# Kernel optimization log

Hardware: AMD Instinct MI355X
Metric: run time of the kernel (lower is better)

## Reference

```python
import jax, jax.numpy as jnp
import numpy as np

N_NODES = 50000
N_EDGES = 800000
IN_DIM = 64
HID = 128
N_LAYERS = 3
NEG_SLOPE = 0.2  # PyG GATConv default


def setup_inputs() -> dict:
    key = jax.random.key(0)
    ks = jax.random.split(key, 24)

    def lin(kw, kb, fan_in, fan_out):
        bound = 1.0 / np.sqrt(fan_in)
        W = jax.random.uniform(kw, (fan_out, fan_in), jnp.float32, -bound, bound)
        b = jax.random.uniform(kb, (fan_out,), jnp.float32, -bound, bound)
        return W, b

    x = jax.random.normal(ks[0], (N_NODES, IN_DIM), jnp.float32)
    h = jax.random.normal(ks[1], (N_NODES, HID), jnp.float32)
    edge_index = jax.random.randint(ks[2], (2, N_EDGES), 0, N_NODES, jnp.int64)

    W_enc, b_enc = lin(ks[3], ks[4], IN_DIM + HID, HID)

    # GAT layer params, stacked over layers: W [L,H,H], att vectors [L,H], bias [L,H]
    Wg = jnp.stack([lin(ks[5 + i], ks[8 + i], HID, HID)[0] for i in range(N_LAYERS)])
    att_src = jax.random.normal(ks[11], (N_LAYERS, HID), jnp.float32) * (1.0 / np.sqrt(HID))
    att_dst = jax.random.normal(ks[12], (N_LAYERS, HID), jnp.float32) * (1.0 / np.sqrt(HID))
    bg = jnp.zeros((N_LAYERS, HID), jnp.float32)

    Wd, bd = lin(ks[13], ks[14], 2 * HID, HID)
    Wd1, bd1 = lin(ks[15], ks[16], HID, HID)
    Wh, bh = lin(ks[17], ks[18], HID, 1)
    Wt, bt = lin(ks[19], ks[20], HID, 1)

    return dict(x=x, h=h, edge_index=edge_index, W_enc=W_enc, b_enc=b_enc,
                Wg=Wg, att_src=att_src, att_dst=att_dst, bg=bg,
                Wd=Wd, bd=bd, Wd1=Wd1, bd1=bd1, Wh=Wh, bh=bh, Wt=Wt, bt=bt)


def _gat_conv(xf, src, dst, W, a_s, a_d, b, n_nodes):
    # xf: [N,H]; messages flow src -> dst, softmax over incoming edges of dst
    xw = xf @ W.T                                   # [N,H]
    e = jax.nn.leaky_relu((xw @ a_s)[src] + (xw @ a_d)[dst], NEG_SLOPE)  # [E]
    m = jax.ops.segment_max(e, dst, num_segments=n_nodes)
    ex = jnp.exp(e - m[dst])
    denom = jax.ops.segment_sum(ex, dst, num_segments=n_nodes)
    alpha = ex / denom[dst]                         # [E]
    out = jax.ops.segment_sum(xw[src] * alpha[:, None], dst, num_segments=n_nodes)
    return out + b


def reference(x, h, edge_index, W_enc, b_enc, Wg, att_src, att_dst, bg,
              Wd, bd, Wd1, bd1, Wh, bh, Wt, bt):
    n = x.shape[0]
    # Encoder
    z = jnp.concatenate([x, h], axis=1) @ W_enc.T + b_enc   # [N,H]

    # add self-loops (PyG GATConv default add_self_loops=True)
    loops = jnp.arange(n, dtype=edge_index.dtype)
    src = jnp.concatenate([edge_index[0], loops])
    dst = jnp.concatenate([edge_index[1], loops])

    # GAT processor: relu(conv_i) for all layers, then last conv applied again (no relu)
    out = z
    for i in range(Wg.shape[0]):
        out = jax.nn.relu(_gat_conv(out, src, dst, Wg[i], att_src[i], att_dst[i], bg[i], n))
    hL = _gat_conv(out, src, dst, Wg[-1], att_src[-1], att_dst[-1], bg[-1], n)

    # Decoder (BatchNorm1d is defined but unused in the original forward)
    d = jax.nn.relu(jnp.concatenate([hL, z], axis=1) @ Wd.T + bd)
    d = jax.nn.relu(d @ Wd1.T + bd1)
    y = jax.nn.sigmoid(d @ Wh.T + bh)                        # [N,1]

    # Termination
    h_bar = jnp.mean(hL, axis=0)                             # [H]
    t = jax.nn.sigmoid(h_bar @ Wt.T + bt)                    # [1]
    return (y, t, hL)
```

## Files before the change

kernel.cpp:

```cpp
#include <hip/hip_runtime.h>

#define N_NODES 50000
#define N_EDGES 800000
#define E_TOT   (N_EDGES + N_NODES)
#define HID     128

typedef unsigned short u16;
typedef unsigned int   u32;
typedef __bf16 bf16x8 __attribute__((ext_vector_type(8)));
typedef float  f32x4  __attribute__((ext_vector_type(4)));

__device__ __forceinline__ float b2f(u16 u) {
  union { u32 i; float f; } c; c.i = ((u32)u) << 16; return c.f;
}
__device__ __forceinline__ u16 f2b(float f) {
  union { float f; u32 i; } c; c.f = f;
  u32 u = c.i;
  return (u16)((u + 0x7fffu + ((u >> 16) & 1u)) >> 16);
}


__global__ void k_detect(const void* x, const void* ei, int* flags) {
  int lane = threadIdx.x;
  const u16* xw = (const u16*)x;
  int wildF = 0;
  #pragma unroll
  for (int i = 0; i < 4; ++i) {
    u16 w = xw[lane + 64 * i];
    int e = (w >> 7) & 0xff;
    if (e >= 0x89) wildF = 1;
  }
  unsigned long long bF = __ballot(wildF);
  const int* e32 = (const int*)ei;
  int nzOdd = 0;
  #pragma unroll
  for (int i = 0; i < 2; ++i)
    if (e32[2 * (lane + 64 * i) + 1] != 0) nzOdd = 1;
  unsigned long long bI = __ballot(nzOdd);
  if (lane == 0) {
    flags[0] = (bF != 0ull) ? 1 : 0;
    flags[1] = (bI != 0ull) ? 0 : 1;
  }
}


__global__ __launch_bounds__(256) void k_convert(
    const void* Wenc, const void* Wg, const void* Wd, const void* Wd1,
    const void* benc, const void* bg, const void* atts, const void* attd,
    const void* bd, const void* bd1, const void* Wh, const void* bh,
    const void* Wt, const void* bt,
    u16* WencH, u16* WencL, u16* WgH, u16* WgL, u16* WdH, u16* WdL,
    u16* Wd1H, u16* Wd1L, float* vecf, const int* flags)
{
  int isF32 = flags[0];
  int t = blockIdx.x * 256 + threadIdx.x;
  auto ld = [&](const void* p, int i) -> float {
    return isF32 ? ((const float*)p)[i] : b2f(((const u16*)p)[i]);
  };
  auto sp = [&](u16* H, u16* L, int i, float v) {
    u16 hh = f2b(v); H[i] = hh; L[i] = f2b(v - b2f(hh));
  };
  if      (t < 24576)  { sp(WencH, WencL, t, ld(Wenc, t)); }
  else if (t < 73728)  { int i = t - 24576;  sp(WgH,  WgL,  i, ld(Wg, i)); }
  else if (t < 106496) { int i = t - 73728;  sp(WdH,  WdL,  i, ld(Wd, i)); }
  else if (t < 122880) { int i = t - 106496; sp(Wd1H, Wd1L, i, ld(Wd1, i)); }
  else if (t < 123008) { int i = t - 122880; vecf[i]        = ld(benc, i); }
  else if (t < 123392) { int i = t - 123008; vecf[128 + i]  = ld(bg, i); }
  else if (t < 123776) { int i = t - 123392; vecf[512 + i]  = ld(atts, i); }
  else if (t < 124160) { int i = t - 123776; vecf[896 + i]  = ld(attd, i); }
  else if (t < 124288) { int i = t - 124160; vecf[1280 + i] = ld(bd, i); }
  else if (t < 124416) { int i = t - 124288; vecf[1408 + i] = ld(bd1, i); }
  else if (t < 124544) { int i = t - 124416; vecf[1536 + i] = ld(Wh, i); }
  else if (t == 124544) { vecf[1664] = ld(bh, 0); }
  else if (t < 124673) { int i = t - 124545; vecf[1665 + i] = ld(Wt, i); }
  else if (t == 124673) { vecf[1793] = ld(bt, 0); }
}


__device__ __forceinline__ int ld_ei(const int* ei, size_t idx, int i64) {
  int v = i64 ? (int)((const long long*)ei)[idx] : ei[idx];
  return ((unsigned)v < (unsigned)N_NODES) ? v : 0;
}

__global__ void k_deg(const int* __restrict__ ei, int* __restrict__ deg, const int* flags) {
  int i64 = flags[1];
  int k = blockIdx.x * 256 + threadIdx.x;
  if (k >= E_TOT) return;
  int d = (k < N_EDGES) ? ld_ei(ei, (size_t)N_EDGES + k, i64) : (k - N_EDGES);
  atomicAdd(&deg[d], 1);
}

__device__ __forceinline__ int block_scan_excl(int v, int lane, int w, int* wsum, int& total) {
  int x = v;
  #pragma unroll
  for (int d = 1; d < 64; d <<= 1) {
    int y = __shfl_up(x, d);
    if (lane >= d) x += y;
  }
  if (lane == 63) wsum[w] = x;
  __syncthreads();
  int wOff = 0;
  #pragma unroll
  for (int i = 0; i < 4; ++i) wOff += (i < w) ? wsum[i] : 0;
  total = wsum[0] + wsum[1] + wsum[2] + wsum[3];
  return wOff + x - v;
}

__global__ void k_scan_block(const int* __restrict__ in, int* __restrict__ outExcl,
                             int* __restrict__ blkSum, int n, int* __restrict__ totalOut) {
  __shared__ int wsum[4];
  int t = threadIdx.x, lane = t & 63, w = t >> 6;
  int gid = blockIdx.x * 256 + t;
  int v = (gid < n) ? in[gid] : 0;
  int total;
  int excl = block_scan_excl(v, lane, w, wsum, total);
  if (gid < n) outExcl[gid] = excl;
  if (t == 0) {
    if (blkSum)   blkSum[blockIdx.x] = total;
    if (totalOut) totalOut[0] = total;
  }
}

__global__ void k_scan_add(int* __restrict__ rowp, const int* __restrict__ blkOff,
                           int* __restrict__ cursor, int n) {
  int gid = blockIdx.x * 256 + threadIdx.x;
  if (gid < n) {
    int r = rowp[gid] + blkOff[blockIdx.x];
    rowp[gid] = r;
    cursor[gid] = r;
  }
}

__global__ void k_scatter(const int* __restrict__ ei, int* __restrict__ cursor,
                          int* __restrict__ colsrc, const int* flags) {
  int i64 = flags[1];
  int k = blockIdx.x * 256 + threadIdx.x;
  if (k >= E_TOT) return;
  int s, d;
  if (k < N_EDGES) { s = ld_ei(ei, k, i64); d = ld_ei(ei, (size_t)N_EDGES + k, i64); }
  else             { s = d = k - N_EDGES; }
  int pos = atomicAdd(&cursor[d], 1);
  colsrc[pos] = s;
}


__device__ __forceinline__ void loadSplit8(const float* p, bf16x8& hi, bf16x8& lo) {
  union { u16 a[8]; bf16x8 v; } H, L;
  #pragma unroll
  for (int i = 0; i < 8; ++i) {
    float v = p[i];
    u16 hh = f2b(v);
    H.a[i] = hh;
    L.a[i] = f2b(v - b2f(hh));
  }
  hi = H.v; lo = L.v;
}

__global__ __launch_bounds__(256) void k_gemm(
    const void* A1a, const void* A1b, int s1, int K1,
    const void* A2a, const void* A2b, int s2,
    const u16* __restrict__ WH, const u16* __restrict__ WL,
    const float* __restrict__ biasF,
    float* __restrict__ outF_, u16* __restrict__ outH, u16* __restrict__ outL,
    const float* __restrict__ asv, const float* __restrict__ adv,
    float* __restrict__ ssrc, float* __restrict__ sdst,
    int N, int K, int relu, int aMode, const int* flags)
{
  int isF32 = flags[0];
  int wid  = blockIdx.x * 4 + (threadIdx.x >> 6);
  int lane = threadIdx.x & 63;
  int q = lane >> 4, c = lane & 15;
  int nb = wid * 32;
  if (nb >= N) return;
  f32x4 acc[2][8] = {};
  int r0 = nb + c;      if (r0 > N - 1) r0 = N - 1;
  int r1 = nb + 16 + c; if (r1 > N - 1) r1 = N - 1;

  for (int kb = 0; kb < K; kb += 32) {
    int kf = kb + q * 8;
    bf16x8 a0h, a1h, a0l, a1l;
    if (aMode == 1) {
      const void* Ap; int stride, ks;
      if (kf < K1) { Ap = A1a; stride = s1; ks = kf; }
      else         { Ap = A2a; stride = s2; ks = kf - K1; }
      if (isF32) {
        loadSplit8((const float*)Ap + (size_t)r0 * stride + ks, a0h, a0l);
        loadSplit8((const float*)Ap + (size_t)r1 * stride + ks, a1h, a1l);
      } else {
        union { u16 u[8]; bf16x8 v; } Z = {};
        a0h = *(const bf16x8*)((const u16*)Ap + (size_t)r0 * stride + ks);
        a1h = *(const bf16x8*)((const u16*)Ap + (size_t)r1 * stride + ks);
        a0l = Z.v; a1l = Z.v;
      }
    } else {
      const u16 *PH, *PL; int stride, ks;
      if (kf < K1) { PH = (const u16*)A1a; PL = (const u16*)A1b; stride = s1; ks = kf; }
      else         { PH = (const u16*)A2a; PL = (const u16*)A2b; stride = s2; ks = kf - K1; }
      a0h = *(const bf16x8*)(PH + (size_t)r0 * stride + ks);
      a0l = *(const bf16x8*)(PL + (size_t)r0 * stride + ks);
      a1h = *(const bf16x8*)(PH + (size_t)r1 * stride + ks);
      a1l = *(const bf16x8*)(PL + (size_t)r1 * stride + ks);
    }
    const u16* wph = WH + (size_t)c * K + kb + q * 8;
    const u16* wpl = WL + (size_t)c * K + kb + q * 8;
    #pragma unroll
    for (int ct = 0; ct < 8; ++ct) {
      bf16x8 bh_ = *(const bf16x8*)(wph + (size_t)(ct * 16) * K);
      bf16x8 bl_ = *(const bf16x8*)(wpl + (size_t)(ct * 16) * K);
      acc[0][ct] = __builtin_amdgcn_mfma_f32_16x16x32_bf16(a0h, bh_, acc[0][ct], 0, 0, 0);
      acc[1][ct] = __builtin_amdgcn_mfma_f32_16x16x32_bf16(a1h, bh_, acc[1][ct], 0, 0, 0);
      acc[0][ct] = __builtin_amdgcn_mfma_f32_16x16x32_bf16(a0h, bl_, acc[0][ct], 0, 0, 0);
      acc[1][ct] = __builtin_amdgcn_mfma_f32_16x16x32_bf16(a1h, bl_, acc[1][ct], 0, 0, 0);
      acc[0][ct] = __builtin_amdgcn_mfma_f32_16x16x32_bf16(a0l, bh_, acc[0][ct], 0, 0, 0);
      acc[1][ct] = __builtin_amdgcn_mfma_f32_16x16x32_bf16(a1l, bh_, acc[1][ct], 0, 0, 0);
    }
  }

  #pragma unroll
  for (int ct = 0; ct < 8; ++ct) {
    int col = ct * 16 + c;
    float bv = biasF ? biasF[col] : 0.0f;
    #pragma unroll
    for (int g = 0; g < 2; ++g) {
      #pragma unroll
      for (int r = 0; r < 4; ++r) {
        float vv = acc[g][ct][r] + bv;
        if (relu) vv = fmaxf(vv, 0.0f);
        acc[g][ct][r] = vv;
        int node = nb + g * 16 + q * 4 + r;
        if (node < N) {
          size_t o = (size_t)node * HID + col;
          if (outF_) outF_[o] = vv;
          if (outH) {
            u16 hh = f2b(vv);
            outH[o] = hh;
            outL[o] = f2b(vv - b2f(hh));
          }
        }
      }
    }
  }

  if (asv) {
    #pragma unroll
    for (int g = 0; g < 2; ++g) {
      #pragma unroll
      for (int r = 0; r < 4; ++r) {
        float ssum = 0.0f, dsum = 0.0f;
        #pragma unroll
        for (int ct = 0; ct < 8; ++ct) {
          int col = ct * 16 + c;
          float v = acc[g][ct][r];
          ssum += v * asv[col];
          dsum += v * adv[col];
        }
        #pragma unroll
        for (int m = 1; m < 16; m <<= 1) {
          ssum += __shfl_xor(ssum, m);
          dsum += __shfl_xor(dsum, m);
        }
        int node = nb + g * 16 + q * 4 + r;
        if (c == 0 && node < N) { ssrc[node] = ssum; sdst[node] = dsum; }
      }
    }
  }
}


__global__ __launch_bounds__(256) void k_softmax(const int* __restrict__ rowp,
    const int* __restrict__ colsrc, const float* __restrict__ ssrc,
    const float* __restrict__ sdst, float* __restrict__ alpha)
{
  int node = blockIdx.x * 4 + (threadIdx.x >> 6);
  int lane = threadIdx.x & 63;
  int start = rowp[node], end = rowp[node + 1];
  float sdv = sdst[node];
  float mx = -1e30f;
  for (int j = start + lane; j < end; j += 64) {
    float e = ssrc[colsrc[j]] + sdv;
    e = (e >= 0.0f) ? e : 0.2f * e;
    alpha[j] = e;
    mx = fmaxf(mx, e);
  }
  #pragma unroll
  for (int d = 1; d < 64; d <<= 1) mx = fmaxf(mx, __shfl_xor(mx, d));
  float sum = 0.0f;
  for (int j = start + lane; j < end; j += 64) {
    float ex = __expf(alpha[j] - mx);
    alpha[j] = ex;
    sum += ex;
  }
  #pragma unroll
  for (int d = 1; d < 64; d <<= 1) sum += __shfl_xor(sum, d);
  float inv = 1.0f / sum;
  for (int j = start + lane; j < end; j += 64) alpha[j] *= inv;
}


__global__ __launch_bounds__(256) void k_gather(const int* __restrict__ rowp,
    const int* __restrict__ colsrc, const float* __restrict__ alpha,
    const float* __restrict__ xw, const float* __restrict__ biasF,
    u16* __restrict__ outH, u16* __restrict__ outL,
    float* __restrict__ out2, int relu)
{
  int node = blockIdx.x * 4 + (threadIdx.x >> 6);
  int lane = threadIdx.x & 63;
  int half = lane >> 5, hl = lane & 31;
  int start = rowp[node], end = rowp[node + 1];
  float a0 = 0, a1 = 0, a2 = 0, a3 = 0;
  for (int j0 = start; j0 < end; j0 += 8) {
    int idx = j0 + (lane & 7);
    bool ok = idx < end;
    int   sI = ok ? colsrc[idx] : 0;
    float aI = ok ? alpha[idx]  : 0.0f;
    #pragma unroll
    for (int t = 0; t < 8; t += 2) {
      int   ss = __shfl(sI, t + half);
      float aa = __shfl(aI, t + half);
      float4 p = *(const float4*)(xw + (size_t)ss * HID + hl * 4);
      a0 += aa * p.x; a1 += aa * p.y; a2 += aa * p.z; a3 += aa * p.w;
    }
  }
  a0 += __shfl_xor(a0, 32); a1 += __shfl_xor(a1, 32);
  a2 += __shfl_xor(a2, 32); a3 += __shfl_xor(a3, 32);
  if (half == 0) {
    int col = hl * 4;
    float4 b = *(const float4*)(biasF + col);
    a0 += b.x; a1 += b.y; a2 += b.z; a3 += b.w;
    if (relu) { a0 = fmaxf(a0, 0.f); a1 = fmaxf(a1, 0.f); a2 = fmaxf(a2, 0.f); a3 = fmaxf(a3, 0.f); }
    size_t o = (size_t)node * HID + col;
    u16 h0 = f2b(a0), h1 = f2b(a1), h2 = f2b(a2), h3 = f2b(a3);
    ushort4 hv; hv.x = h0; hv.y = h1; hv.z = h2; hv.w = h3;
    *(ushort4*)(outH + o) = hv;
    ushort4 lv;
    lv.x = f2b(a0 - b2f(h0)); lv.y = f2b(a1 - b2f(h1));
    lv.z = f2b(a2 - b2f(h2)); lv.w = f2b(a3 - b2f(h3));
    *(ushort4*)(outL + o) = lv;
    if (out2) { out2[o] = a0; out2[o + 1] = a1; out2[o + 2] = a2; out2[o + 3] = a3; }
  }
}


__global__ __launch_bounds__(256) void k_hbar(const u16* __restrict__ hH, const u16* __restrict__ hLo,
                                              float* __restrict__ hbar) {
  int t = threadIdx.x;
  int col = t & 127, g = t >> 7;
  float acc = 0.0f;
  for (int n = blockIdx.x * 2 + g; n < N_NODES; n += gridDim.x * 2) {
    size_t o = (size_t)n * HID + col;
    acc += b2f(hH[o]) + b2f(hLo[o]);
  }
  atomicAdd(&hbar[col], acc);
}


__global__ __launch_bounds__(256) void k_ydot(const float* __restrict__ d2,
    const float* __restrict__ Whf, const float* __restrict__ bhf, float* __restrict__ yout)
{
  int node = blockIdx.x * 4 + (threadIdx.x >> 6);
  int lane = threadIdx.x & 63;
  float2 p = *(const float2*)(d2 + (size_t)node * HID + lane * 2);
  float v = p.x * Whf[lane * 2] + p.y * Whf[lane * 2 + 1];
  #pragma unroll
  for (int d = 1; d < 64; d <<= 1) v += __shfl_xor(v, d);
  if (lane == 0) {
    float s = 1.0f / (1.0f + __expf(-(v + bhf[0])));
    yout[node] = s;
  }
}


__global__ void k_tker(const float* __restrict__ hbar, const float* __restrict__ Wtf,
                       const float* __restrict__ btf, float* __restrict__ tout) {
  int lane = threadIdx.x;
  float v = hbar[lane] * Wtf[lane] + hbar[lane + 64] * Wtf[lane + 64];
  #pragma unroll
  for (int d = 1; d < 64; d <<= 1) v += __shfl_xor(v, d);
  if (lane == 0) {
    float t = 1.0f / (1.0f + __expf(-(v * (1.0f / N_NODES) + btf[0])));
    tout[0] = t;
  }
}


extern "C" void kernel_launch(void* const* d_in, const int* in_sizes, int n_in,
                              void* d_out, int out_size, void* d_ws, size_t ws_size,
                              hipStream_t stream) {
  const void* x    = d_in[0];
  const void* h    = d_in[1];
  const int*  ei   = (const int*)d_in[2];
  const void* Wenc = d_in[3];
  const void* benc = d_in[4];
  const void* Wg   = d_in[5];
  const void* atts = d_in[6];
  const void* attd = d_in[7];
  const void* bg   = d_in[8];
  const void* Wd   = d_in[9];
  const void* bd   = d_in[10];
  const void* Wd1  = d_in[11];
  const void* bd1v = d_in[12];
  const void* Wh   = d_in[13];
  const void* bh   = d_in[14];
  const void* Wt   = d_in[15];
  const void* bt   = d_in[16];
  float* outF = (float*)d_out;

  char* w = (char*)d_ws;
  auto alloc = [&](size_t bytes) { char* p = w; w += (bytes + 255) & ~(size_t)255; return p; };
  const size_t NPLANE = (size_t)N_NODES * HID;
  float* xwF    = (float*)alloc(NPLANE * 4);
  u16*   zH     = (u16*)  alloc(NPLANE * 2);
  u16*   zL     = (u16*)  alloc(NPLANE * 2);
  u16*   aH     = (u16*)  alloc(NPLANE * 2);
  u16*   aL     = (u16*)  alloc(NPLANE * 2);
  float* ssrc   = (float*)alloc((size_t)N_NODES * 4);
  float* sdst   = (float*)alloc((size_t)N_NODES * 4);
  int*   deg    = (int*)  alloc((size_t)N_NODES * 4);
  int*   rowp   = (int*)  alloc((size_t)(N_NODES + 1) * 4);
  int*   cursor = (int*)  alloc((size_t)N_NODES * 4);
  int*   colsrc = (int*)  alloc((size_t)E_TOT * 4);
  float* alpha  = (float*)alloc((size_t)E_TOT * 4);
  int*   blkSum = (int*)  alloc(1024);
  int*   blkOff = (int*)  alloc(1024);
  float* hbar   = (float*)alloc(512);
  int*   flags  = (int*)  alloc(256);
  u16*   WencH  = (u16*)  alloc(24576 * 2);
  u16*   WencL  = (u16*)  alloc(24576 * 2);
  u16*   WgH    = (u16*)  alloc(49152 * 2);
  u16*   WgL    = (u16*)  alloc(49152 * 2);
  u16*   WdH    = (u16*)  alloc(32768 * 2);
  u16*   WdL    = (u16*)  alloc(32768 * 2);
  u16*   Wd1H   = (u16*)  alloc(16384 * 2);
  u16*   Wd1L   = (u16*)  alloc(16384 * 2);
  float* vecf   = (float*)alloc(2048 * 4);
  u16*   dH     = (u16*)xwF;
  u16*   dL     = dH + NPLANE;
  float* d2F    = (float*)aH;

  const int NODE_BLKS = N_NODES / 4;
  const int EDGE_BLKS = (E_TOT + 255) / 256;
  const int SCAN_BLKS = (N_NODES + 255) / 256;
  const int GEMM_BLKS = ((N_NODES + 31) / 32 + 3) / 4;
  const int CONV_BLKS = (124674 + 255) / 256;

  k_detect<<<1, 64, 0, stream>>>(x, ei, flags);
  k_convert<<<CONV_BLKS, 256, 0, stream>>>(Wenc, Wg, Wd, Wd1, benc, bg, atts, attd,
                                           bd, bd1v, Wh, bh, Wt, bt,
                                           WencH, WencL, WgH, WgL, WdH, WdL,
                                           Wd1H, Wd1L, vecf, flags);

  hipMemsetAsync(deg, 0, (size_t)N_NODES * 4, stream);
  hipMemsetAsync(hbar, 0, 128 * sizeof(float), stream);
  k_deg<<<EDGE_BLKS, 256, 0, stream>>>(ei, deg, flags);
  k_scan_block<<<SCAN_BLKS, 256, 0, stream>>>(deg, rowp, blkSum, N_NODES, nullptr);
  k_scan_block<<<1, 256, 0, stream>>>(blkSum, blkOff, nullptr, SCAN_BLKS, rowp + N_NODES);
  k_scan_add<<<SCAN_BLKS, 256, 0, stream>>>(rowp, blkOff, cursor, N_NODES);
  k_scatter<<<EDGE_BLKS, 256, 0, stream>>>(ei, cursor, colsrc, flags);

  k_gemm<<<GEMM_BLKS, 256, 0, stream>>>(x, nullptr, 64, 64, h, nullptr, HID,
                                        WencH, WencL, vecf,
                                        nullptr, zH, zL,
                                        nullptr, nullptr, nullptr, nullptr,
                                        N_NODES, 192, 0, 1, flags);

  for (int l4 = 0; l4 < 4; ++l4) {
    int l = (l4 < 3) ? l4 : 2;
    int relu = (l4 < 3) ? 1 : 0;
    const u16* inH = (l4 == 0) ? zH : aH;
    const u16* inL = (l4 == 0) ? zL : aL;
    k_gemm<<<GEMM_BLKS, 256, 0, stream>>>(inH, inL, HID, HID, nullptr, nullptr, HID,
                                          WgH + (size_t)l * HID * HID, WgL + (size_t)l * HID * HID,
                                          nullptr,
                                          xwF, nullptr, nullptr,
                                          vecf + 512 + l * HID, vecf + 896 + l * HID, ssrc, sdst,
                                          N_NODES, HID, 0, 2, flags);
    k_softmax<<<NODE_BLKS, 256, 0, stream>>>(rowp, colsrc, ssrc, sdst, alpha);
    k_gather<<<NODE_BLKS, 256, 0, stream>>>(rowp, colsrc, alpha, xwF, vecf + 128 + l * HID,
                                            aH, aL, (l4 == 3) ? (outF + N_NODES + 1) : nullptr, relu);
  }

  k_hbar<<<256, 256, 0, stream>>>(aH, aL, hbar);

  k_gemm<<<GEMM_BLKS, 256, 0, stream>>>(aH, aL, HID, HID, zH, zL, HID,
                                        WdH, WdL, vecf + 1280,
                                        nullptr, dH, dL,
                                        nullptr, nullptr, nullptr, nullptr,
                                        N_NODES, 256, 1, 2, flags);
  k_gemm<<<GEMM_BLKS, 256, 0, stream>>>(dH, dL, HID, HID, nullptr, nullptr, HID,
                                        Wd1H, Wd1L, vecf + 1408,
                                        d2F, nullptr, nullptr,
                                        nullptr, nullptr, nullptr, nullptr,
                                        N_NODES, 128, 1, 2, flags);
  k_ydot<<<NODE_BLKS, 256, 0, stream>>>(d2F, vecf + 1536, vecf + 1664, outF);
  k_tker<<<1, 64, 0, stream>>>(hbar, vecf + 1665, vecf + 1793, outF + N_NODES);
}
```

Measured before the change: 782.9 us.

## Precompute W^T·att vectors and fuse attention scores into gather epilogue

Result: slower. 844.8 us (+7.9%).

```diff
diff --git a/kernel.cpp b/kernel.cpp
--- a/kernel.cpp
+++ b/kernel.cpp
@@ -77,6 +77,21 @@
 }
 
 
+__global__ void k_wa(const u16* __restrict__ WgH, const u16* __restrict__ WgL,
+                     const float* __restrict__ vecf, float* __restrict__ waS, float* __restrict__ waD) {
+  int t = blockIdx.x * 256 + threadIdx.x;
+  if (t >= 768) return;
+  int l = t / 256, sel = (t / 128) & 1, k = t & 127;
+  const float* av = vecf + (sel ? 896 : 512) + l * HID;
+  const u16* H = WgH + (size_t)l * HID * HID;
+  const u16* L = WgL + (size_t)l * HID * HID;
+  float s = 0.0f;
+  for (int c = 0; c < HID; ++c)
+    s += (b2f(H[(size_t)c * HID + k]) + b2f(L[(size_t)c * HID + k])) * av[c];
+  (sel ? waD : waS)[l * HID + k] = s;
+}
+
+
 __device__ __forceinline__ int ld_ei(const int* ei, size_t idx, int i64) {
   int v = i64 ? (int)((const long long*)ei)[idx] : ei[idx];
   return ((unsigned)v < (unsigned)N_NODES) ? v : 0;
@@ -162,8 +177,6 @@
     const u16* __restrict__ WH, const u16* __restrict__ WL,
     const float* __restrict__ biasF,
     float* __restrict__ outF_, u16* __restrict__ outH, u16* __restrict__ outL,
-    const float* __restrict__ asv, const float* __restrict__ adv,
-    float* __restrict__ ssrc, float* __restrict__ sdst,
     int N, int K, int relu, int aMode, const int* flags)
 {
   int isF32 = flags[0];
@@ -226,7 +239,6 @@
       for (int r = 0; r < 4; ++r) {
         float vv = acc[g][ct][r] + bv;
         if (relu) vv = fmaxf(vv, 0.0f);
-        acc[g][ct][r] = vv;
         int node = nb + g * 16 + q * 4 + r;
         if (node < N) {
           size_t o = (size_t)node * HID + col;
@@ -240,30 +252,25 @@
       }
     }
   }
-
-  if (asv) {
-    #pragma unroll
-    for (int g = 0; g < 2; ++g) {
-      #pragma unroll
-      for (int r = 0; r < 4; ++r) {
-        float ssum = 0.0f, dsum = 0.0f;
-        #pragma unroll
-        for (int ct = 0; ct < 8; ++ct) {
-          int col = ct * 16 + c;
-          float v = acc[g][ct][r];
-          ssum += v * asv[col];
-          dsum += v * adv[col];
-        }
-        #pragma unroll
-        for (int m = 1; m < 16; m <<= 1) {
-          ssum += __shfl_xor(ssum, m);
-          dsum += __shfl_xor(dsum, m);
-        }
-        int node = nb + g * 16 + q * 4 + r;
-        if (c == 0 && node < N) { ssrc[node] = ssum; sdst[node] = dsum; }
-      }
-    }
-  }
+}
+
+
+__global__ __launch_bounds__(256) void k_sdots(const u16* __restrict__ zH, const u16* __restrict__ zL,
+    const float* __restrict__ waS0, const float* __restrict__ waD0,
+    float* __restrict__ ssrc, float* __restrict__ sdst)
+{
+  int node = blockIdx.x * 4 + (threadIdx.x >> 6);
+  int lane = threadIdx.x & 63;
+  size_t o = (size_t)node * HID + lane * 2;
+  u32 ph = *(const u32*)(zH + o);
+  u32 pl = *(const u32*)(zL + o);
+  float v0 = b2f((u16)ph) + b2f((u16)pl);
+  float v1 = b2f((u16)(ph >> 16)) + b2f((u16)(pl >> 16));
+  float vs = v0 * waS0[lane * 2] + v1 * waS0[lane * 2 + 1];
+  float vd = v0 * waD0[lane * 2] + v1 * waD0[lane * 2 + 1];
+  #pragma unroll
+  for (int d = 1; d < 64; d <<= 1) { vs += __shfl_xor(vs, d); vd += __shfl_xor(vd, d); }
+  if (lane == 0) { ssrc[node] = vs; sdst[node] = vd; }
 }
 
 
@@ -301,20 +308,23 @@
     const int* __restrict__ colsrc, const float* __restrict__ alpha,
     const float* __restrict__ xw, const float* __restrict__ biasF,
     u16* __restrict__ outH, u16* __restrict__ outL,
-    float* __restrict__ out2, int relu)
+    float* __restrict__ out2,
+    const float* __restrict__ waSn, const float* __restrict__ waDn,
+    float* __restrict__ ssrc, float* __restrict__ sdst, int relu)
 {
   int node = blockIdx.x * 4 + (threadIdx.x >> 6);
   int lane = threadIdx.x & 63;
   int half = lane >> 5, hl = lane & 31;
   int start = rowp[node], end = rowp[node + 1];
   float a0 = 0, a1 = 0, a2 = 0, a3 = 0;
-  for (int j0 = start; j0 < end; j0 += 8) {
-    int idx = j0 + (lane & 7);
+  for (int j0 = start; j0 < end; j0 += 16) {
+    int idx = j0 + (lane & 15);
     bool ok = idx < end;
     int   sI = ok ? colsrc[idx] : 0;
     float aI = ok ? alpha[idx]  : 0.0f;
     #pragma unroll
-    for (int t = 0; t < 8; t += 2) {
+    for (int t = 0; t < 16; t += 2) {
+      if (j0 + t >= end) break;
       int   ss = __shfl(sI, t + half);
       float aa = __shfl(aI, t + half);
       float4 p = *(const float4*)(xw + (size_t)ss * HID + hl * 4);
@@ -323,11 +333,11 @@
   }
   a0 += __shfl_xor(a0, 32); a1 += __shfl_xor(a1, 32);
   a2 += __shfl_xor(a2, 32); a3 += __shfl_xor(a3, 32);
+  int col = hl * 4;
+  float4 b = *(const float4*)(biasF + col);
+  a0 += b.x; a1 += b.y; a2 += b.z; a3 += b.w;
+  if (relu) { a0 = fmaxf(a0, 0.f); a1 = fmaxf(a1, 0.f); a2 = fmaxf(a2, 0.f); a3 = fmaxf(a3, 0.f); }
   if (half == 0) {
-    int col = hl * 4;
-    float4 b = *(const float4*)(biasF + col);
-    a0 += b.x; a1 += b.y; a2 += b.z; a3 += b.w;
-    if (relu) { a0 = fmaxf(a0, 0.f); a1 = fmaxf(a1, 0.f); a2 = fmaxf(a2, 0.f); a3 = fmaxf(a3, 0.f); }
     size_t o = (size_t)node * HID + col;
     u16 h0 = f2b(a0), h1 = f2b(a1), h2 = f2b(a2), h3 = f2b(a3);
     ushort4 hv; hv.x = h0; hv.y = h1; hv.z = h2; hv.w = h3;
@@ -337,6 +347,15 @@
     lv.z = f2b(a2 - b2f(h2)); lv.w = f2b(a3 - b2f(h3));
     *(ushort4*)(outL + o) = lv;
     if (out2) { out2[o] = a0; out2[o + 1] = a1; out2[o + 2] = a2; out2[o + 3] = a3; }
+  }
+  if (waSn) {
+    float4 ws = *(const float4*)(waSn + col);
+    float4 wd = *(const float4*)(waDn + col);
+    float vs = a0 * ws.x + a1 * ws.y + a2 * ws.z + a3 * ws.w;
+    float vd = a0 * wd.x + a1 * wd.y + a2 * wd.z + a3 * wd.w;
+    #pragma unroll
+    for (int d = 1; d < 32; d <<= 1) { vs += __shfl_xor(vs, d); vd += __shfl_xor(vd, d); }
+    if (lane == 0) { ssrc[node] = vs; sdst[node] = vd; }
   }
 }
 
@@ -433,6 +452,8 @@
   u16*   Wd1H   = (u16*)  alloc(16384 * 2);
   u16*   Wd1L   = (u16*)  alloc(16384 * 2);
   float* vecf   = (float*)alloc(2048 * 4);
+  float* waS    = (float*)alloc(3 * HID * 4);
+  float* waD    = (float*)alloc(3 * HID * 4);
   u16*   dH     = (u16*)xwF;
   u16*   dL     = dH + NPLANE;
   float* d2F    = (float*)aH;
@@ -448,6 +469,7 @@
                                            bd, bd1v, Wh, bh, Wt, bt,
                                            WencH, WencL, WgH, WgL, WdH, WdL,
                                            Wd1H, Wd1L, vecf, flags);
+  k_wa<<<3, 256, 0, stream>>>(WgH, WgL, vecf, waS, waD);
 
   hipMemsetAsync(deg, 0, (size_t)N_NODES * 4, stream);
   hipMemsetAsync(hbar, 0, 128 * sizeof(float), stream);
@@ -460,23 +482,26 @@
   k_gemm<<<GEMM_BLKS, 256, 0, stream>>>(x, nullptr, 64, 64, h, nullptr, HID,
                                         WencH, WencL, vecf,
                                         nullptr, zH, zL,
-                                        nullptr, nullptr, nullptr, nullptr,
                                         N_NODES, 192, 0, 1, flags);
+  k_sdots<<<NODE_BLKS, 256, 0, stream>>>(zH, zL, waS, waD, ssrc, sdst);
 
   for (int l4 = 0; l4 < 4; ++l4) {
     int l = (l4 < 3) ? l4 : 2;
     int relu = (l4 < 3) ? 1 : 0;
+    int lnext = (l4 + 1 < 3) ? (l4 + 1) : 2;
     const u16* inH = (l4 == 0) ? zH : aH;
     const u16* inL = (l4 == 0) ? zL : aL;
     k_gemm<<<GEMM_BLKS, 256, 0, stream>>>(inH, inL, HID, HID, nullptr, nullptr, HID,
                                           WgH + (size_t)l * HID * HID, WgL + (size_t)l * HID * HID,
                                           nullptr,
                                           xwF, nullptr, nullptr,
-                                          vecf + 512 + l * HID, vecf + 896 + l * HID, ssrc, sdst,
                                           N_NODES, HID, 0, 2, flags);
     k_softmax<<<NODE_BLKS, 256, 0, stream>>>(rowp, colsrc, ssrc, sdst, alpha);
     k_gather<<<NODE_BLKS, 256, 0, stream>>>(rowp, colsrc, alpha, xwF, vecf + 128 + l * HID,
-                                            aH, aL, (l4 == 3) ? (outF + N_NODES + 1) : nullptr, relu);
+                                            aH, aL, (l4 == 3) ? (outF + N_NODES + 1) : nullptr,
+                                            (l4 < 3) ? (waS + lnext * HID) : nullptr,
+                                            (l4 < 3) ? (waD + lnext * HID) : nullptr,
+                                            ssrc, sdst, relu);
   }
 
   k_hbar<<<256, 256, 0, stream>>>(aH, aL, hbar);
@@ -484,12 +509,10 @@
   k_gemm<<<GEMM_BLKS, 256, 0, stream>>>(aH, aL, HID, HID, zH, zL, HID,
                                         WdH, WdL, vecf + 1280,
                                         nullptr, dH, dL,
-                                        nullptr, nullptr, nullptr, nullptr,
                                         N_NODES, 256, 1, 2, flags);
   k_gemm<<<GEMM_BLKS, 256, 0, stream>>>(dH, dL, HID, HID, nullptr, nullptr, HID,
                                         Wd1H, Wd1L, vecf + 1408,
                                         d2F, nullptr, nullptr,
-                                        nullptr, nullptr, nullptr, nullptr,
                                         N_NODES, 128, 1, 2, flags);
   k_ydot<<<NODE_BLKS, 256, 0, stream>>>(d2F, vecf + 1536, vecf + 1664, outF);
   k_tker<<<1, 64, 0, stream>>>(hbar, vecf + 1665, vecf + 1793, outF + N_NODES);
```

## Fuse edge softmax into gather kernel, recomputing attention weights in registers

Applied to the files above, without the earlier changes.

Result: faster. 719.9 us (-8.0%).

```diff
diff --git a/kernel.cpp b/kernel.cpp
--- a/kernel.cpp
+++ b/kernel.cpp
@@ -267,39 +267,10 @@
 }
 
 
-__global__ __launch_bounds__(256) void k_softmax(const int* __restrict__ rowp,
+__global__ __launch_bounds__(256) void k_fused(const int* __restrict__ rowp,
     const int* __restrict__ colsrc, const float* __restrict__ ssrc,
-    const float* __restrict__ sdst, float* __restrict__ alpha)
-{
-  int node = blockIdx.x * 4 + (threadIdx.x >> 6);
-  int lane = threadIdx.x & 63;
-  int start = rowp[node], end = rowp[node + 1];
-  float sdv = sdst[node];
-  float mx = -1e30f;
-  for (int j = start + lane; j < end; j += 64) {
-    float e = ssrc[colsrc[j]] + sdv;
-    e = (e >= 0.0f) ? e : 0.2f * e;
-    alpha[j] = e;
-    mx = fmaxf(mx, e);
-  }
-  #pragma unroll
-  for (int d = 1; d < 64; d <<= 1) mx = fmaxf(mx, __shfl_xor(mx, d));
-  float sum = 0.0f;
-  for (int j = start + lane; j < end; j += 64) {
-    float ex = __expf(alpha[j] - mx);
-    alpha[j] = ex;
-    sum += ex;
-  }
-  #pragma unroll
-  for (int d = 1; d < 64; d <<= 1) sum += __shfl_xor(sum, d);
-  float inv = 1.0f / sum;
-  for (int j = start + lane; j < end; j += 64) alpha[j] *= inv;
-}
-
-
-__global__ __launch_bounds__(256) void k_gather(const int* __restrict__ rowp,
-    const int* __restrict__ colsrc, const float* __restrict__ alpha,
-    const float* __restrict__ xw, const float* __restrict__ biasF,
+    const float* __restrict__ sdst, const float* __restrict__ xw,
+    const float* __restrict__ biasF,
     u16* __restrict__ outH, u16* __restrict__ outL,
     float* __restrict__ out2, int relu)
 {
@@ -307,16 +278,55 @@
   int lane = threadIdx.x & 63;
   int half = lane >> 5, hl = lane & 31;
   int start = rowp[node], end = rowp[node + 1];
+  float sdv = sdst[node];
+
+  int jC = start + lane;
+  bool okC = jC < end;
+  int   sC = okC ? colsrc[jC] : 0;
+  float eC = -1e30f;
+  if (okC) {
+    float e = ssrc[sC] + sdv;
+    eC = (e >= 0.0f) ? e : 0.2f * e;
+  }
+  float mx = eC;
+  for (int j = start + 64 + lane; j < end; j += 64) {
+    float e = ssrc[colsrc[j]] + sdv;
+    e = (e >= 0.0f) ? e : 0.2f * e;
+    mx = fmaxf(mx, e);
+  }
+  #pragma unroll
+  for (int d = 1; d < 64; d <<= 1) mx = fmaxf(mx, __shfl_xor(mx, d));
+
+  float sum = okC ? __expf(eC - mx) : 0.0f;
+  for (int j = start + 64 + lane; j < end; j += 64) {
+    float e = ssrc[colsrc[j]] + sdv;
+    e = (e >= 0.0f) ? e : 0.2f * e;
+    sum += __expf(e - mx);
+  }
+  #pragma unroll
+  for (int d = 1; d < 64; d <<= 1) sum += __shfl_xor(sum, d);
+  float inv = 1.0f / sum;
+  float alC = okC ? __expf(eC - mx) * inv : 0.0f;
+
   float a0 = 0, a1 = 0, a2 = 0, a3 = 0;
   for (int j0 = start; j0 < end; j0 += 8) {
-    int idx = j0 + (lane & 7);
-    bool ok = idx < end;
-    int   sI = ok ? colsrc[idx] : 0;
-    float aI = ok ? alpha[idx]  : 0.0f;
+    int base = j0 - start;
+    int   sI; float aI;
+    if (base < 64) {
+      sI = sC; aI = alC;
+    } else {
+      int idx = j0 + (lane & 7);
+      bool ok = idx < end;
+      sI = ok ? colsrc[idx] : 0;
+      float e = ok ? (ssrc[sI] + sdv) : 0.0f;
+      e = (e >= 0.0f) ? e : 0.2f * e;
+      aI = ok ? __expf(e - mx) * inv : 0.0f;
+    }
+    int src = (base < 64) ? base : 0;
     #pragma unroll
     for (int t = 0; t < 8; t += 2) {
-      int   ss = __shfl(sI, t + half);
-      float aa = __shfl(aI, t + half);
+      int   ss = __shfl(sI, src + t + half);
+      float aa = __shfl(aI, src + t + half);
       float4 p = *(const float4*)(xw + (size_t)ss * HID + hl * 4);
       a0 += aa * p.x; a1 += aa * p.y; a2 += aa * p.z; a3 += aa * p.w;
     }
@@ -419,7 +429,6 @@
   int*   rowp   = (int*)  alloc((size_t)(N_NODES + 1) * 4);
   int*   cursor = (int*)  alloc((size_t)N_NODES * 4);
   int*   colsrc = (int*)  alloc((size_t)E_TOT * 4);
-  float* alpha  = (float*)alloc((size_t)E_TOT * 4);
   int*   blkSum = (int*)  alloc(1024);
   int*   blkOff = (int*)  alloc(1024);
   float* hbar   = (float*)alloc(512);
@@ -474,9 +483,8 @@
                                           xwF, nullptr, nullptr,
                                           vecf + 512 + l * HID, vecf + 896 + l * HID, ssrc, sdst,
                                           N_NODES, HID, 0, 2, flags);
-    k_softmax<<<NODE_BLKS, 256, 0, stream>>>(rowp, colsrc, ssrc, sdst, alpha);
-    k_gather<<<NODE_BLKS, 256, 0, stream>>>(rowp, colsrc, alpha, xwF, vecf + 128 + l * HID,
-                                            aH, aL, (l4 == 3) ? (outF + N_NODES + 1) : nullptr, relu);
+    k_fused<<<NODE_BLKS, 256, 0, stream>>>(rowp, colsrc, ssrc, sdst, xwF, vecf + 128 + l * HID,
+                                           aH, aL, (l4 == 3) ? (outF + N_NODES + 1) : nullptr, relu);
   }
 
   k_hbar<<<256, 256, 0, stream>>>(aH, aL, hbar);
```
